# Optimization experiments

Hardware: AMD Instinct MI355X
Metric: run time of the kernel (lower is better)

Reference implementation:

```python
import jax, jax.numpy as jnp
import numpy as np
import math

N_NODES = 100000
N_EDGES = 1600000
D_FEAT = 32
K = 1        # Bernstein index k
N_ORD = 2    # Bernstein order n
COMB = float(math.comb(N_ORD, K))


def setup_inputs() -> dict:
    key = jax.random.key(0)
    k1, k2, k3 = jax.random.split(key, 3)
    feat = jax.random.normal(k1, (N_NODES, D_FEAT), dtype=jnp.float32)
    edge_src = jax.random.randint(k2, (N_EDGES,), 0, N_NODES)
    edge_dst = jax.random.randint(k3, (N_EDGES,), 0, N_NODES)
    return {"feat": feat, "edge_src": edge_src, "edge_dst": edge_dst}


def reference(feat, edge_src, edge_dst):
    # in-degree of each node (copy_u/sum aggregates over incoming edges)
    deg = jax.ops.segment_sum(jnp.ones((N_EDGES,), feat.dtype), edge_dst,
                              num_segments=N_NODES)
    d_invsqrt = jnp.clip(deg, 1.0, None) ** -0.5  # [N]
    d_invsqrt = d_invsqrt[:, None]                 # [N,1]

    def unn_laplacian(x):
        msg = (x * d_invsqrt)[edge_src]            # [E,D]
        agg = jax.ops.segment_sum(msg, edge_dst, num_segments=N_NODES)
        return x - agg * d_invsqrt

    if K == 0:
        h = feat
        for _ in range(N_ORD):
            h = unn_laplacian(h) / 2
            h = feat - h
    elif K == N_ORD:
        h = feat
        for _ in range(N_ORD):
            h = unn_laplacian(h) / 2
    else:
        temp = feat
        for _ in range(K):
            temp = unn_laplacian(temp) / 2
        h = feat
        for _ in range(N_ORD - K):
            h = unn_laplacian(h) / 2
            h = feat - h
        h = temp * h
    return COMB * h
```

## Files before the change

kernel.cpp:

```cpp
#include <hip/hip_runtime.h>

#define N_NODES 100000
#define N_EDGES 1600000
#define D_FEAT 32

#define BSH 7
#define BMASK 127
#define NB 782
#define CAPB 2432

#define P1_BS 1024
#define P1_TILE 4096
#define P1_CAP 16


typedef float v4f __attribute__((ext_vector_type(4)));

static __device__ __forceinline__ unsigned pack_bf16(float a, float b) {
    unsigned ua = __float_as_uint(a);
    unsigned ub = __float_as_uint(b);
    ua = (ua + 0x7FFFu + ((ua >> 16) & 1u)) >> 16;
    ub = (ub + 0x7FFFu + ((ub >> 16) & 1u)) >> 16;
    return (ua & 0xFFFFu) | (ub << 16);
}

__global__ void init_kernel(int* __restrict__ cursorA) {
    int b = blockIdx.x * blockDim.x + threadIdx.x;
    if (b < NB) cursorA[b] = b * CAPB;
}

__global__ void __launch_bounds__(P1_BS)
bucket_kernel(const int* __restrict__ edge_src,
              const int* __restrict__ edge_dst,
              int* __restrict__ cursorA,
              int* __restrict__ pairs, int n_edges) {
    __shared__ int s_cnt[NB];
    __shared__ int s_base[NB];
    __shared__ int s_buf[NB * P1_CAP];

    int tile = blockIdx.x * P1_TILE;
    if (tile >= n_edges) return;

    for (int b = threadIdx.x; b < NB; b += P1_BS) s_cnt[b] = 0;
    __syncthreads();

    const int4* src4 = reinterpret_cast<const int4*>(edge_src);
    const int4* dst4 = reinterpret_cast<const int4*>(edge_dst);
    int tileq = blockIdx.x * (P1_TILE / 4);
    {
        int iq = tileq + threadIdx.x;
        if (iq * 4 < n_edges) {
            int4 sv = src4[iq];
            int4 dv = dst4[iq];
            int ss[4] = {sv.x, sv.y, sv.z, sv.w};
            int dd[4] = {dv.x, dv.y, dv.z, dv.w};
            #pragma unroll
            for (int u = 0; u < 4; ++u) {
                int b = dd[u] >> BSH;
                int packed = (ss[u] << BSH) | (dd[u] & BMASK);
                int p = atomicAdd(&s_cnt[b], 1);
                if (p < P1_CAP) {
                    s_buf[b * P1_CAP + p] = packed;
                } else {
                    int gp = atomicAdd(&cursorA[b], 1);
                    pairs[gp] = packed;
                }
            }
        }
    }
    __syncthreads();

    for (int b = threadIdx.x; b < NB; b += P1_BS) {
        int c = min(s_cnt[b], P1_CAP);
        s_cnt[b] = c;
        s_base[b] = atomicAdd(&cursorA[b], c);
    }
    __syncthreads();

    for (int idx = threadIdx.x; idx < NB * P1_CAP; idx += P1_BS) {
        int b = idx >> 4;
        int slot = idx & (P1_CAP - 1);
        if (slot < s_cnt[b])
            pairs[s_base[b] + slot] = s_buf[idx];
    }
}

__global__ void __launch_bounds__(512)
prep_kernel(const int* __restrict__ pairs,
            const int* __restrict__ cursorA,
            const float* __restrict__ feat,
            unsigned* __restrict__ sfeat) {
    __shared__ int h[128];
    __shared__ float dv_s[128];

    int b = blockIdx.x;
    int t = threadIdx.x;
    int base = b * CAPB;
    int cnt = min(cursorA[b] - base, CAPB);

    if (t < 128) h[t] = 0;
    __syncthreads();
    for (int i = t; i < cnt; i += 512)
        atomicAdd(&h[pairs[base + i] & BMASK], 1);
    __syncthreads();

    if (t < 128)
        dv_s[t] = rsqrtf(fmaxf((float)h[t], 1.0f));
    __syncthreads();

    const float4* feat4 = reinterpret_cast<const float4*>(feat);
    uint4* sf4 = reinterpret_cast<uint4*>(sfeat);
    for (int idx = t; idx < 128 * 4; idx += 512) {
        int nl = idx >> 2;
        int q = idx & 3;
        int node = (b << BSH) + nl;
        if (node >= N_NODES) continue;
        float dvv = dv_s[nl];
        float4 fa = feat4[node * 8 + 2 * q];
        float4 fb = feat4[node * 8 + 2 * q + 1];
        uint4 pk;
        pk.x = pack_bf16(fa.x * dvv, fa.y * dvv);
        pk.y = pack_bf16(fa.z * dvv, fa.w * dvv);
        pk.z = pack_bf16(fb.x * dvv, fb.y * dvv);
        pk.w = pack_bf16(fb.z * dvv, fb.w * dvv);
        sf4[node * 4 + q] = pk;
    }
}

__global__ void __launch_bounds__(512)
sortgather_kernel(const int* __restrict__ pairs,
                  const int* __restrict__ cursorA,
                  const float* __restrict__ feat,
                  const unsigned* __restrict__ sfeat,
                  float* __restrict__ out) {
    __shared__ int buf[CAPB];
    __shared__ int outb[CAPB];
    __shared__ int h[128];
    __shared__ int sc[128];
    __shared__ int cur[128];
    __shared__ float dv_s[128];

    int b = blockIdx.x;
    int t = threadIdx.x;
    int base = b * CAPB;
    int cnt = min(cursorA[b] - base, CAPB);

    if (t < 128) h[t] = 0;
    __syncthreads();
    for (int i = t; i < cnt; i += 512) {
        int p = pairs[base + i];
        buf[i] = p;
        atomicAdd(&h[p & BMASK], 1);
    }
    __syncthreads();

    if (t < 64) {
        int a  = h[2 * t];
        int b2 = h[2 * t + 1];
        int s = a + b2;
        #pragma unroll
        for (int off = 1; off < 64; off <<= 1) {
            int x = __shfl_up(s, off);
            if (t >= off) s += x;
        }
        sc[2 * t]     = s - b2;
        sc[2 * t + 1] = s;
    }
    __syncthreads();
    if (t < 128) {
        cur[t] = sc[t] - h[t];
        dv_s[t] = rsqrtf(fmaxf((float)h[t], 1.0f));
    }
    __syncthreads();

    for (int i = t; i < cnt; i += 512) {
        int p = buf[i];
        int pos = atomicAdd(&cur[p & BMASK], 1);
        outb[pos] = p >> BSH;
    }
    __syncthreads();

    const uint4* sf4 = reinterpret_cast<const uint4*>(sfeat);
    const v4f* featv = reinterpret_cast<const v4f*>(feat);
    v4f* outv = reinterpret_cast<v4f*>(out);

    {
        int nl = t >> 2;
        int q = t & 3;
        int node = (b << BSH) + nl;
        if (node < N_NODES) {
            int en = sc[nl];
            int k = en - h[nl];
            float a0 = 0.f, a1 = 0.f, a2 = 0.f, a3 = 0.f;
            float a4 = 0.f, a5 = 0.f, a6 = 0.f, a7 = 0.f;

            #define ACC(r)                                                 \
                a0 += __uint_as_float((r).x << 16);                        \
                a1 += __uint_as_float((r).x & 0xFFFF0000u);                \
                a2 += __uint_as_float((r).y << 16);                        \
                a3 += __uint_as_float((r).y & 0xFFFF0000u);                \
                a4 += __uint_as_float((r).z << 16);                        \
                a5 += __uint_as_float((r).z & 0xFFFF0000u);                \
                a6 += __uint_as_float((r).w << 16);                        \
                a7 += __uint_as_float((r).w & 0xFFFF0000u);

            for (; k + 7 < en; k += 8) {
                int s0 = outb[k],     s1 = outb[k + 1];
                int s2 = outb[k + 2], s3 = outb[k + 3];
                int s4 = outb[k + 4], s5 = outb[k + 5];
                int s6 = outb[k + 6], s7 = outb[k + 7];
                uint4 r0 = sf4[s0 * 4 + q];
                uint4 r1 = sf4[s1 * 4 + q];
                uint4 r2 = sf4[s2 * 4 + q];
                uint4 r3 = sf4[s3 * 4 + q];
                uint4 r4 = sf4[s4 * 4 + q];
                uint4 r5 = sf4[s5 * 4 + q];
                uint4 r6 = sf4[s6 * 4 + q];
                uint4 r7 = sf4[s7 * 4 + q];
                ACC(r0) ACC(r1) ACC(r2) ACC(r3)
                ACC(r4) ACC(r5) ACC(r6) ACC(r7)
            }
            for (; k + 3 < en; k += 4) {
                int s0 = outb[k],     s1 = outb[k + 1];
                int s2 = outb[k + 2], s3 = outb[k + 3];
                uint4 r0 = sf4[s0 * 4 + q];
                uint4 r1 = sf4[s1 * 4 + q];
                uint4 r2 = sf4[s2 * 4 + q];
                uint4 r3 = sf4[s3 * 4 + q];
                ACC(r0) ACC(r1) ACC(r2) ACC(r3)
            }
            for (; k < en; ++k) {
                uint4 r = sf4[outb[k] * 4 + q];
                ACC(r)
            }
            #undef ACC

            float dvn = dv_s[nl];
            v4f fa = __builtin_nontemporal_load(&featv[node * 8 + 2 * q]);
            v4f fb = __builtin_nontemporal_load(&featv[node * 8 + 2 * q + 1]);
            v4f oa, ob;
            float y;
            y = 0.5f * (fa.x - a0 * dvn); oa.x = 2.0f * y * (fa.x - y);
            y = 0.5f * (fa.y - a1 * dvn); oa.y = 2.0f * y * (fa.y - y);
            y = 0.5f * (fa.z - a2 * dvn); oa.z = 2.0f * y * (fa.z - y);
            y = 0.5f * (fa.w - a3 * dvn); oa.w = 2.0f * y * (fa.w - y);
            y = 0.5f * (fb.x - a4 * dvn); ob.x = 2.0f * y * (fb.x - y);
            y = 0.5f * (fb.y - a5 * dvn); ob.y = 2.0f * y * (fb.y - y);
            y = 0.5f * (fb.z - a6 * dvn); ob.z = 2.0f * y * (fb.z - y);
            y = 0.5f * (fb.w - a7 * dvn); ob.w = 2.0f * y * (fb.w - y);
            __builtin_nontemporal_store(oa, &outv[node * 8 + 2 * q]);
            __builtin_nontemporal_store(ob, &outv[node * 8 + 2 * q + 1]);
        }
    }
}

extern "C" void kernel_launch(void* const* d_in, const int* in_sizes, int n_in,
                              void* d_out, int out_size, void* d_ws, size_t ws_size,
                              hipStream_t stream) {
    const float* feat = (const float*)d_in[0];
    const int* edge_src = (const int*)d_in[1];
    const int* edge_dst = (const int*)d_in[2];
    float* out = (float*)d_out;

    int* ws = (int*)d_ws;
    int* cursorA    = ws;
    int* pairs      = cursorA + 1024;
    unsigned* sfeat = (unsigned*)(pairs + NB * CAPB);

    init_kernel<<<1, 1024, 0, stream>>>(cursorA);
    {
        int blocks = (N_EDGES + P1_TILE - 1) / P1_TILE;
        bucket_kernel<<<blocks, P1_BS, 0, stream>>>(edge_src, edge_dst,
                                                    cursorA, pairs, N_EDGES);
    }
    prep_kernel<<<NB, 512, 0, stream>>>(pairs, cursorA, feat, sfeat);
    sortgather_kernel<<<NB, 512, 0, stream>>>(pairs, cursorA, feat, sfeat, out);
}
```

Before: 113.1 us.

## Replace global atomic bucket cursors with fixed per-tile slots and overflow area

The bucketing pass now writes each tile's per-bucket edges into a fixed slot region indexed by (bucket, tile), with a byte count per cell, instead of reserving space through global atomic cursors. Only edges beyond 16 per cell go to a small per-bucket overflow array through global atomics. The prep and sort-gather kernels scan all 391 tile cells per bucket, using the count bytes to skip empty slots. This removes most global atomic contention, at the cost of reading a sparse, padded cell array and adding a capped overflow path that drops edges if a bucket's overflow exceeds 32 entries.

```diff
diff --git a/kernel.cpp b/kernel.cpp
--- a/kernel.cpp
+++ b/kernel.cpp
@@ -7,11 +7,13 @@
 #define BSH 7
 #define BMASK 127
 #define NB 782
-#define CAPB 2432
+#define NT 391
+#define SLOT 16
+#define OVF_CAP 32
+#define CAPB_MAX 2432
 
 #define P1_BS 1024
 #define P1_TILE 4096
-#define P1_CAP 16
 
 
 typedef float v4f __attribute__((ext_vector_type(4)));
@@ -24,84 +26,87 @@
     return (ua & 0xFFFFu) | (ub << 16);
 }
 
-__global__ void init_kernel(int* __restrict__ cursorA) {
+__global__ void init_kernel(int* __restrict__ ovfcur) {
     int b = blockIdx.x * blockDim.x + threadIdx.x;
-    if (b < NB) cursorA[b] = b * CAPB;
+    if (b < 1024) ovfcur[b] = b * OVF_CAP;
 }
 
 __global__ void __launch_bounds__(P1_BS)
 bucket_kernel(const int* __restrict__ edge_src,
               const int* __restrict__ edge_dst,
-              int* __restrict__ cursorA,
-              int* __restrict__ pairs, int n_edges) {
+              int* __restrict__ ovfcur,
+              int* __restrict__ ovf,
+              int* __restrict__ pairs2,
+              unsigned char* __restrict__ cnt8, int n_edges) {
     __shared__ int s_cnt[NB];
-    __shared__ int s_base[NB];
-    __shared__ int s_buf[NB * P1_CAP];
-
-    int tile = blockIdx.x * P1_TILE;
-    if (tile >= n_edges) return;
-
-    for (int b = threadIdx.x; b < NB; b += P1_BS) s_cnt[b] = 0;
+    __shared__ int s_buf[NB * SLOT];
+
+    int T = blockIdx.x;
+    int t = threadIdx.x;
+
+    for (int b = t; b < NB; b += P1_BS) s_cnt[b] = 0;
     __syncthreads();
 
     const int4* src4 = reinterpret_cast<const int4*>(edge_src);
     const int4* dst4 = reinterpret_cast<const int4*>(edge_dst);
-    int tileq = blockIdx.x * (P1_TILE / 4);
-    {
-        int iq = tileq + threadIdx.x;
-        if (iq * 4 < n_edges) {
-            int4 sv = src4[iq];
-            int4 dv = dst4[iq];
-            int ss[4] = {sv.x, sv.y, sv.z, sv.w};
-            int dd[4] = {dv.x, dv.y, dv.z, dv.w};
-            #pragma unroll
-            for (int u = 0; u < 4; ++u) {
-                int b = dd[u] >> BSH;
-                int packed = (ss[u] << BSH) | (dd[u] & BMASK);
-                int p = atomicAdd(&s_cnt[b], 1);
-                if (p < P1_CAP) {
-                    s_buf[b * P1_CAP + p] = packed;
-                } else {
-                    int gp = atomicAdd(&cursorA[b], 1);
-                    pairs[gp] = packed;
-                }
+    int iq = T * (P1_TILE / 4) + t;
+    if (iq * 4 < n_edges) {
+        int4 sv = src4[iq];
+        int4 dv = dst4[iq];
+        int ss[4] = {sv.x, sv.y, sv.z, sv.w};
+        int dd[4] = {dv.x, dv.y, dv.z, dv.w};
+        #pragma unroll
+        for (int u = 0; u < 4; ++u) {
+            int b = dd[u] >> BSH;
+            int packed = (ss[u] << BSH) | (dd[u] & BMASK);
+            int p = atomicAdd(&s_cnt[b], 1);
+            if (p < SLOT) {
+                s_buf[b * SLOT + p] = packed;
+            } else {
+                int gp = atomicAdd(&ovfcur[b], 1);
+                ovf[gp] = packed;
             }
         }
     }
     __syncthreads();
 
-    for (int b = threadIdx.x; b < NB; b += P1_BS) {
-        int c = min(s_cnt[b], P1_CAP);
-        s_cnt[b] = c;
-        s_base[b] = atomicAdd(&cursorA[b], c);
-    }
-    __syncthreads();
-
-    for (int idx = threadIdx.x; idx < NB * P1_CAP; idx += P1_BS) {
+    for (int idx = t; idx < NB * SLOT; idx += P1_BS) {
         int b = idx >> 4;
-        int slot = idx & (P1_CAP - 1);
-        if (slot < s_cnt[b])
-            pairs[s_base[b] + slot] = s_buf[idx];
-    }
+        int slot = idx & (SLOT - 1);
+        if (slot < min(s_cnt[b], SLOT))
+            pairs2[(b * NT + T) * SLOT + slot] = s_buf[idx];
+    }
+    for (int b = t; b < NB; b += P1_BS)
+        cnt8[T * NB + b] = (unsigned char)min(s_cnt[b], SLOT);
 }
 
 __global__ void __launch_bounds__(512)
-prep_kernel(const int* __restrict__ pairs,
-            const int* __restrict__ cursorA,
+prep_kernel(const int* __restrict__ pairs2,
+            const unsigned char* __restrict__ cnt8,
+            const int* __restrict__ ovfcur,
+            const int* __restrict__ ovf,
             const float* __restrict__ feat,
             unsigned* __restrict__ sfeat) {
     __shared__ int h[128];
     __shared__ float dv_s[128];
+    __shared__ unsigned char sc8[NT];
 
     int b = blockIdx.x;
     int t = threadIdx.x;
-    int base = b * CAPB;
-    int cnt = min(cursorA[b] - base, CAPB);
 
     if (t < 128) h[t] = 0;
-    __syncthreads();
-    for (int i = t; i < cnt; i += 512)
-        atomicAdd(&h[pairs[base + i] & BMASK], 1);
+    for (int i = t; i < NT; i += 512) sc8[i] = cnt8[i * NB + b];
+    __syncthreads();
+
+    const int* cellbase = pairs2 + b * (NT * SLOT);
+    for (int i = t; i < NT * SLOT; i += 512) {
+        int T = i >> 4, s = i & (SLOT - 1);
+        if (s < (int)sc8[T])
+            atomicAdd(&h[cellbase[i] & BMASK], 1);
+    }
+    int ocnt = ovfcur[b] - b * OVF_CAP;
+    for (int i = t; i < ocnt; i += 512)
+        atomicAdd(&h[ovf[b * OVF_CAP + i] & BMASK], 1);
     __syncthreads();
 
     if (t < 128)
@@ -128,13 +133,15 @@
 }
 
 __global__ void __launch_bounds__(512)
-sortgather_kernel(const int* __restrict__ pairs,
-                  const int* __restrict__ cursorA,
+sortgather_kernel(const int* __restrict__ pairs2,
+                  const unsigned char* __restrict__ cnt8,
+                  const int* __restrict__ ovfcur,
+                  const int* __restrict__ ovf,
                   const float* __restrict__ feat,
                   const unsigned* __restrict__ sfeat,
                   float* __restrict__ out) {
-    __shared__ int buf[CAPB];
-    __shared__ int outb[CAPB];
+    __shared__ int outb[CAPB_MAX];
+    __shared__ unsigned char sc8[NT];
     __shared__ int h[128];
     __shared__ int sc[128];
     __shared__ int cur[128];
@@ -142,16 +149,20 @@
 
     int b = blockIdx.x;
     int t = threadIdx.x;
-    int base = b * CAPB;
-    int cnt = min(cursorA[b] - base, CAPB);
 
     if (t < 128) h[t] = 0;
-    __syncthreads();
-    for (int i = t; i < cnt; i += 512) {
-        int p = pairs[base + i];
-        buf[i] = p;
-        atomicAdd(&h[p & BMASK], 1);
-    }
+    for (int i = t; i < NT; i += 512) sc8[i] = cnt8[i * NB + b];
+    __syncthreads();
+
+    const int* cellbase = pairs2 + b * (NT * SLOT);
+    for (int i = t; i < NT * SLOT; i += 512) {
+        int T = i >> 4, s = i & (SLOT - 1);
+        if (s < (int)sc8[T])
+            atomicAdd(&h[cellbase[i] & BMASK], 1);
+    }
+    int ocnt = ovfcur[b] - b * OVF_CAP;
+    for (int i = t; i < ocnt; i += 512)
+        atomicAdd(&h[ovf[b * OVF_CAP + i] & BMASK], 1);
     __syncthreads();
 
     if (t < 64) {
@@ -173,10 +184,18 @@
     }
     __syncthreads();
 
-    for (int i = t; i < cnt; i += 512) {
-        int p = buf[i];
+    for (int i = t; i < NT * SLOT; i += 512) {
+        int T = i >> 4, s = i & (SLOT - 1);
+        if (s < (int)sc8[T]) {
+            int p = cellbase[i];
+            int pos = atomicAdd(&cur[p & BMASK], 1);
+            if (pos < CAPB_MAX) outb[pos] = p >> BSH;
+        }
+    }
+    for (int i = t; i < ocnt; i += 512) {
+        int p = ovf[b * OVF_CAP + i];
         int pos = atomicAdd(&cur[p & BMASK], 1);
-        outb[pos] = p >> BSH;
+        if (pos < CAPB_MAX) outb[pos] = p >> BSH;
     }
     __syncthreads();
 
@@ -184,73 +203,71 @@
     const v4f* featv = reinterpret_cast<const v4f*>(feat);
     v4f* outv = reinterpret_cast<v4f*>(out);
 
-    {
-        int nl = t >> 2;
-        int q = t & 3;
-        int node = (b << BSH) + nl;
-        if (node < N_NODES) {
-            int en = sc[nl];
-            int k = en - h[nl];
-            float a0 = 0.f, a1 = 0.f, a2 = 0.f, a3 = 0.f;
-            float a4 = 0.f, a5 = 0.f, a6 = 0.f, a7 = 0.f;
-
-            #define ACC(r)                                                 \
-                a0 += __uint_as_float((r).x << 16);                        \
-                a1 += __uint_as_float((r).x & 0xFFFF0000u);                \
-                a2 += __uint_as_float((r).y << 16);                        \
-                a3 += __uint_as_float((r).y & 0xFFFF0000u);                \
-                a4 += __uint_as_float((r).z << 16);                        \
-                a5 += __uint_as_float((r).z & 0xFFFF0000u);                \
-                a6 += __uint_as_float((r).w << 16);                        \
-                a7 += __uint_as_float((r).w & 0xFFFF0000u);
-
-            for (; k + 7 < en; k += 8) {
-                int s0 = outb[k],     s1 = outb[k + 1];
-                int s2 = outb[k + 2], s3 = outb[k + 3];
-                int s4 = outb[k + 4], s5 = outb[k + 5];
-                int s6 = outb[k + 6], s7 = outb[k + 7];
-                uint4 r0 = sf4[s0 * 4 + q];
-                uint4 r1 = sf4[s1 * 4 + q];
-                uint4 r2 = sf4[s2 * 4 + q];
-                uint4 r3 = sf4[s3 * 4 + q];
-                uint4 r4 = sf4[s4 * 4 + q];
-                uint4 r5 = sf4[s5 * 4 + q];
-                uint4 r6 = sf4[s6 * 4 + q];
-                uint4 r7 = sf4[s7 * 4 + q];
-                ACC(r0) ACC(r1) ACC(r2) ACC(r3)
-                ACC(r4) ACC(r5) ACC(r6) ACC(r7)
-            }
-            for (; k + 3 < en; k += 4) {
-                int s0 = outb[k],     s1 = outb[k + 1];
-                int s2 = outb[k + 2], s3 = outb[k + 3];
-                uint4 r0 = sf4[s0 * 4 + q];
-                uint4 r1 = sf4[s1 * 4 + q];
-                uint4 r2 = sf4[s2 * 4 + q];
-                uint4 r3 = sf4[s3 * 4 + q];
-                ACC(r0) ACC(r1) ACC(r2) ACC(r3)
-            }
-            for (; k < en; ++k) {
-                uint4 r = sf4[outb[k] * 4 + q];
-                ACC(r)
-            }
-            #undef ACC
-
-            float dvn = dv_s[nl];
-            v4f fa = __builtin_nontemporal_load(&featv[node * 8 + 2 * q]);
-            v4f fb = __builtin_nontemporal_load(&featv[node * 8 + 2 * q + 1]);
-            v4f oa, ob;
-            float y;
-            y = 0.5f * (fa.x - a0 * dvn); oa.x = 2.0f * y * (fa.x - y);
-            y = 0.5f * (fa.y - a1 * dvn); oa.y = 2.0f * y * (fa.y - y);
-            y = 0.5f * (fa.z - a2 * dvn); oa.z = 2.0f * y * (fa.z - y);
-            y = 0.5f * (fa.w - a3 * dvn); oa.w = 2.0f * y * (fa.w - y);
-            y = 0.5f * (fb.x - a4 * dvn); ob.x = 2.0f * y * (fb.x - y);
-            y = 0.5f * (fb.y - a5 * dvn); ob.y = 2.0f * y * (fb.y - y);
-            y = 0.5f * (fb.z - a6 * dvn); ob.z = 2.0f * y * (fb.z - y);
-            y = 0.5f * (fb.w - a7 * dvn); ob.w = 2.0f * y * (fb.w - y);
-            __builtin_nontemporal_store(oa, &outv[node * 8 + 2 * q]);
-            __builtin_nontemporal_store(ob, &outv[node * 8 + 2 * q + 1]);
-        }
+    int nl = t >> 2;
+    int q = t & 3;
+    int node = (b << BSH) + nl;
+    if (node < N_NODES) {
+        int en = min(sc[nl], CAPB_MAX);
+        int k = max(en - h[nl], 0);
+        float a0 = 0.f, a1 = 0.f, a2 = 0.f, a3 = 0.f;
+        float a4 = 0.f, a5 = 0.f, a6 = 0.f, a7 = 0.f;
+
+        #define ACC(r)                                                 \
+            a0 += __uint_as_float((r).x << 16);                        \
+            a1 += __uint_as_float((r).x & 0xFFFF0000u);                \
+            a2 += __uint_as_float((r).y << 16);                        \
+            a3 += __uint_as_float((r).y & 0xFFFF0000u);                \
+            a4 += __uint_as_float((r).z << 16);                        \
+            a5 += __uint_as_float((r).z & 0xFFFF0000u);                \
+            a6 += __uint_as_float((r).w << 16);                        \
+            a7 += __uint_as_float((r).w & 0xFFFF0000u);
+
+        for (; k + 7 < en; k += 8) {
+            int s0 = outb[k],     s1 = outb[k + 1];
+            int s2 = outb[k + 2], s3 = outb[k + 3];
+            int s4 = outb[k + 4], s5 = outb[k + 5];
+            int s6 = outb[k + 6], s7 = outb[k + 7];
+            uint4 r0 = sf4[s0 * 4 + q];
+            uint4 r1 = sf4[s1 * 4 + q];
+            uint4 r2 = sf4[s2 * 4 + q];
+            uint4 r3 = sf4[s3 * 4 + q];
+            uint4 r4 = sf4[s4 * 4 + q];
+            uint4 r5 = sf4[s5 * 4 + q];
+            uint4 r6 = sf4[s6 * 4 + q];
+            uint4 r7 = sf4[s7 * 4 + q];
+            ACC(r0) ACC(r1) ACC(r2) ACC(r3)
+            ACC(r4) ACC(r5) ACC(r6) ACC(r7)
+        }
+        for (; k + 3 < en; k += 4) {
+            int s0 = outb[k],     s1 = outb[k + 1];
+            int s2 = outb[k + 2], s3 = outb[k + 3];
+            uint4 r0 = sf4[s0 * 4 + q];
+            uint4 r1 = sf4[s1 * 4 + q];
+            uint4 r2 = sf4[s2 * 4 + q];
+            uint4 r3 = sf4[s3 * 4 + q];
+            ACC(r0) ACC(r1) ACC(r2) ACC(r3)
+        }
+        for (; k < en; ++k) {
+            uint4 r = sf4[outb[k] * 4 + q];
+            ACC(r)
+        }
+        #undef ACC
+
+        float dvn = dv_s[nl];
+        v4f fa = __builtin_nontemporal_load(&featv[node * 8 + 2 * q]);
+        v4f fb = __builtin_nontemporal_load(&featv[node * 8 + 2 * q + 1]);
+        v4f oa, ob;
+        float y;
+        y = 0.5f * (fa.x - a0 * dvn); oa.x = 2.0f * y * (fa.x - y);
+        y = 0.5f * (fa.y - a1 * dvn); oa.y = 2.0f * y * (fa.y - y);
+        y = 0.5f * (fa.z - a2 * dvn); oa.z = 2.0f * y * (fa.z - y);
+        y = 0.5f * (fa.w - a3 * dvn); oa.w = 2.0f * y * (fa.w - y);
+        y = 0.5f * (fb.x - a4 * dvn); ob.x = 2.0f * y * (fb.x - y);
+        y = 0.5f * (fb.y - a5 * dvn); ob.y = 2.0f * y * (fb.y - y);
+        y = 0.5f * (fb.z - a6 * dvn); ob.z = 2.0f * y * (fb.z - y);
+        y = 0.5f * (fb.w - a7 * dvn); ob.w = 2.0f * y * (fb.w - y);
+        __builtin_nontemporal_store(oa, &outv[node * 8 + 2 * q]);
+        __builtin_nontemporal_store(ob, &outv[node * 8 + 2 * q + 1]);
     }
 }
 
@@ -263,16 +280,17 @@
     float* out = (float*)d_out;
 
     int* ws = (int*)d_ws;
-    int* cursorA    = ws;
-    int* pairs      = cursorA + 1024;
-    unsigned* sfeat = (unsigned*)(pairs + NB * CAPB);
-
-    init_kernel<<<1, 1024, 0, stream>>>(cursorA);
-    {
-        int blocks = (N_EDGES + P1_TILE - 1) / P1_TILE;
-        bucket_kernel<<<blocks, P1_BS, 0, stream>>>(edge_src, edge_dst,
-                                                    cursorA, pairs, N_EDGES);
-    }
-    prep_kernel<<<NB, 512, 0, stream>>>(pairs, cursorA, feat, sfeat);
-    sortgather_kernel<<<NB, 512, 0, stream>>>(pairs, cursorA, feat, sfeat, out);
-}
+    int* ovfcur = ws;
+    int* ovf    = ovfcur + 1024;
+    int* pairs2 = ovf + NB * OVF_CAP;
+    unsigned char* cnt8 = (unsigned char*)(pairs2 + NB * NT * SLOT);
+    size_t cnt8_pad = ((size_t)NT * NB + 15) & ~(size_t)15;
+    unsigned* sfeat = (unsigned*)(cnt8 + cnt8_pad);
+
+    init_kernel<<<1, 1024, 0, stream>>>(ovfcur);
+    bucket_kernel<<<NT, P1_BS, 0, stream>>>(edge_src, edge_dst, ovfcur, ovf,
+                                            pairs2, cnt8, N_EDGES);
+    prep_kernel<<<NB, 512, 0, stream>>>(pairs2, cnt8, ovfcur, ovf, feat, sfeat);
+    sortgather_kernel<<<NB, 512, 0, stream>>>(pairs2, cnt8, ovfcur, ovf,
+                                              feat, sfeat, out);
+}
```

Measured after the change: 128.1 us. 13.2% more time.
